# Kernel tuning notes

Measured on AMD Instinct MI355X. Metric: run time of the kernel, lower is better.

The kernel has to match this reference:

```python
import jax, jax.numpy as jnp
import numpy as np

B, C, HID, H, W_ = 16, 2048, 256, 32, 32

def setup_inputs() -> dict:
    key = jax.random.key(0)
    k1, k2, k3 = jax.random.split(key, 3)
    return {
        "query_features": jax.random.normal(k1, (B, C, H, W_), dtype=jnp.float32),
        "prompt_features": jax.random.normal(k2, (B, C, H, W_), dtype=jnp.float32),
        "W": jax.random.normal(k3, (HID, C), dtype=jnp.float32) * 0.02,
        "b": jnp.zeros((HID,), dtype=jnp.float32),
    }

def reference(query_features, prompt_features, W, b):
    Bq, Cc, Hh, Ww = query_features.shape
    HW = Hh * Ww
    # 1x1 conv == channel matmul
    Q = jnp.einsum('oc,bchw->bohw', W, query_features) + b[None, :, None, None]
    K = jnp.einsum('oc,bchw->bohw', W, prompt_features) + b[None, :, None, None]
    Qf = Q.reshape(Bq, -1, HW)          # (b, hid, HW1)
    Kf = K.reshape(Bq, -1, HW)          # (b, hid, HW2)
    Vf = prompt_features.reshape(Bq, Cc, HW)  # (b, C, HW2)
    scores = jnp.einsum('bcq,bck->bqk', Qf, Kf)   # (b, HW1, HW2)
    A = jax.nn.softmax(scores, axis=-1)
    aligned = jnp.einsum('bqk,bck->bcq', A, Vf).reshape(Bq, Cc, Hh, Ww)
    # fusion_policy == 'cat'
    return jnp.concatenate([query_features, aligned], axis=1)
```

## Files before the change

kernel.cpp:

```cpp
#include <hip/hip_runtime.h>

#define NB   16
#define NC   2048
#define NHID 256
#define NHW  1024
#define ROWH 36

using half4_t  = __attribute__((ext_vector_type(4))) _Float16;
using half8_t  = __attribute__((ext_vector_type(8))) _Float16;
using float4_t = __attribute__((ext_vector_type(4))) float;

__global__ __launch_bounds__(256) void copy_kernel(const uint4* __restrict__ qf,
                                                   uint4* __restrict__ out) {
    int idx = blockIdx.x * 256 + threadIdx.x;
    int b = idx >> 19;
    int r = idx & 0x7FFFF;
    out[((size_t)b << 20) + r] = qf[idx];
}

__device__ __forceinline__ void stage_f32(const float* __restrict__ src, size_t stride,
                                          int k0, _Float16* __restrict__ dst, int t) {
    #pragma unroll
    for (int i = 0; i < 4; ++i) {
        int flat = i * 256 + t;
        int row = flat >> 3;
        int ch  = flat & 7;
        float4 v = *(const float4*)(src + (size_t)row * stride + k0 + ch * 4);
        half4_t h;
        h[0] = (_Float16)v.x; h[1] = (_Float16)v.y;
        h[2] = (_Float16)v.z; h[3] = (_Float16)v.w;
        *(half4_t*)(dst + row * ROWH + ch * 4) = h;
    }
}

__device__ __forceinline__ void stage_f16(const _Float16* __restrict__ src, size_t stride,
                                          int k0, _Float16* __restrict__ dst, int t) {
    #pragma unroll
    for (int i = 0; i < 2; ++i) {
        int flat = i * 256 + t;
        int row = flat >> 2;
        int ch  = flat & 3;
        const _Float16* p = src + (size_t)row * stride + k0 + ch * 8;
        half4_t h0 = *(const half4_t*)p;
        half4_t h1 = *(const half4_t*)(p + 4);
        *(half4_t*)(dst + row * ROWH + ch * 8)     = h0;
        *(half4_t*)(dst + row * ROWH + ch * 8 + 4) = h1;
    }
}

__device__ __forceinline__ void stage_f32_T(const float* __restrict__ src, size_t stride,
                                            int k0, _Float16* __restrict__ dst, int t) {
    const int j = t & 31;
    const int g = t >> 5;
    float4 xr[4];
    #pragma unroll
    for (int r = 0; r < 4; ++r)
        xr[r] = *(const float4*)(src + (size_t)(k0 + g * 4 + r) * stride + j * 4);
    #pragma unroll
    for (int e = 0; e < 4; ++e) {
        half4_t h;
        h[0] = (_Float16)((&xr[0].x)[e]);
        h[1] = (_Float16)((&xr[1].x)[e]);
        h[2] = (_Float16)((&xr[2].x)[e]);
        h[3] = (_Float16)((&xr[3].x)[e]);
        *(half4_t*)(dst + (j * 4 + e) * ROWH + g * 4) = h;
    }
}

__device__ __forceinline__ void mfma_step(const _Float16* __restrict__ As,
                                          const _Float16* __restrict__ Bs,
                                          int wr, int wc, int quad, int l15,
                                          float4_t acc[4][4]) {
    half8_t af[4], bf[4];
    #pragma unroll
    for (int i = 0; i < 4; ++i) {
        const _Float16* pa = As + (wr + i * 16 + l15) * ROWH + quad * 8;
        half4_t a0 = *(const half4_t*)pa;
        half4_t a1 = *(const half4_t*)(pa + 4);
        const _Float16* pb = Bs + (wc + i * 16 + l15) * ROWH + quad * 8;
        half4_t b0 = *(const half4_t*)pb;
        half4_t b1 = *(const half4_t*)(pb + 4);
        #pragma unroll
        for (int e = 0; e < 4; ++e) {
            af[i][e] = a0[e]; af[i][4 + e] = a1[e];
            bf[i][e] = b0[e]; bf[i][4 + e] = b1[e];
        }
    }
    #pragma unroll
    for (int i = 0; i < 4; ++i)
        #pragma unroll
        for (int j = 0; j < 4; ++j)
            acc[i][j] = __builtin_amdgcn_mfma_f32_16x16x32_f16(af[i], bf[j], acc[i][j], 0, 0, 0);
}

#define ACC_INIT(acc) \
    _Pragma("unroll") for (int i_ = 0; i_ < 4; ++i_) \
    _Pragma("unroll") for (int j_ = 0; j_ < 4; ++j_) \
    _Pragma("unroll") for (int r_ = 0; r_ < 4; ++r_) acc[i_][j_][r_] = 0.f;

__global__ __launch_bounds__(256) void proj16_kernel(
    const float* __restrict__ qf, const float* __restrict__ pf,
    const float* __restrict__ Wm, const float* __restrict__ bias,
    _Float16* __restrict__ Q16, _Float16* __restrict__ K16)
{
    __shared__ _Float16 As[128 * ROWH];
    __shared__ _Float16 Bs[128 * ROWH];
    const int z = blockIdx.z;
    const int which = z >> 4;
    const int b = z & 15;
    const float* X = (which ? pf : qf) + (size_t)b * NC * NHW;
    _Float16* O = (which ? K16 : Q16) + (size_t)b * NHW * NHID;
    const int m0 = blockIdx.y * 128;
    const int n0 = blockIdx.x * 128;
    const int t = threadIdx.x;
    const int w = t >> 6, l = t & 63, quad = l >> 4, l15 = l & 15;
    const int wr = (w >> 1) * 64, wc = (w & 1) * 64;

    float4_t acc[4][4];
    ACC_INIT(acc)

    for (int k0 = 0; k0 < NC; k0 += 32) {
        stage_f32_T(X + m0, NHW, k0, As, t);
        stage_f32(Wm + (size_t)n0 * NC, NC, k0, Bs, t);
        __syncthreads();
        mfma_step(As, Bs, wr, wc, quad, l15, acc);
        __syncthreads();
    }
    float bv[4];
    #pragma unroll
    for (int j = 0; j < 4; ++j) bv[j] = bias[n0 + wc + j * 16 + l15];
    #pragma unroll
    for (int i = 0; i < 4; ++i)
        #pragma unroll
        for (int j = 0; j < 4; ++j)
            #pragma unroll
            for (int r = 0; r < 4; ++r) {
                int hw  = m0 + wr + i * 16 + quad * 4 + r;
                int hid = n0 + wc + j * 16 + l15;
                O[(size_t)hw * NHID + hid] = (_Float16)(acc[i][j][r] + bv[j]);
            }
}

__global__ __launch_bounds__(256) void scores16_kernel(
    const _Float16* __restrict__ Q16, const _Float16* __restrict__ K16,
    float* __restrict__ S)
{
    __shared__ _Float16 As[128 * ROWH];
    __shared__ _Float16 Bs[128 * ROWH];
    const int b = blockIdx.z;
    const _Float16* Qb = Q16 + (size_t)b * NHW * NHID;
    const _Float16* Kb = K16 + (size_t)b * NHW * NHID;
    float* Sb = S + (size_t)b * NHW * NHW;
    const int m0 = blockIdx.y * 128;
    const int n0 = blockIdx.x * 128;
    const int t = threadIdx.x;
    const int w = t >> 6, l = t & 63, quad = l >> 4, l15 = l & 15;
    const int wr = (w >> 1) * 64, wc = (w & 1) * 64;

    float4_t acc[4][4];
    ACC_INIT(acc)

    for (int k0 = 0; k0 < NHID; k0 += 32) {
        stage_f16(Qb + (size_t)m0 * NHID, NHID, k0, As, t);
        stage_f16(Kb + (size_t)n0 * NHID, NHID, k0, Bs, t);
        __syncthreads();
        mfma_step(As, Bs, wr, wc, quad, l15, acc);
        __syncthreads();
    }
    #pragma unroll
    for (int i = 0; i < 4; ++i)
        #pragma unroll
        for (int j = 0; j < 4; ++j)
            #pragma unroll
            for (int r = 0; r < 4; ++r) {
                int q1 = m0 + wr + i * 16 + quad * 4 + r;
                int q2 = n0 + wc + j * 16 + l15;
                Sb[(size_t)q1 * NHW + q2] = acc[i][j][r];
            }
}

__global__ __launch_bounds__(256) void softmax_kernel(float* __restrict__ S) {
    const int t = threadIdx.x;
    const int wave = t >> 6;
    const int lane = t & 63;
    float* row = S + ((size_t)blockIdx.x * 4 + wave) * NHW;

    float4 v[4];
    float mx = -1e30f;
    #pragma unroll
    for (int j = 0; j < 4; ++j) {
        v[j] = *(const float4*)(row + (lane << 2) + (j << 8));
        mx = fmaxf(mx, fmaxf(fmaxf(v[j].x, v[j].y), fmaxf(v[j].z, v[j].w)));
    }
    #pragma unroll
    for (int off = 32; off >= 1; off >>= 1)
        mx = fmaxf(mx, __shfl_xor(mx, off, 64));

    float s = 0.f;
    #pragma unroll
    for (int j = 0; j < 4; ++j) {
        v[j].x = __expf(v[j].x - mx); v[j].y = __expf(v[j].y - mx);
        v[j].z = __expf(v[j].z - mx); v[j].w = __expf(v[j].w - mx);
        s += v[j].x + v[j].y + v[j].z + v[j].w;
    }
    #pragma unroll
    for (int off = 32; off >= 1; off >>= 1)
        s += __shfl_xor(s, off, 64);

    const float inv = 1.0f / s;
    #pragma unroll
    for (int j = 0; j < 4; ++j) {
        v[j].x *= inv; v[j].y *= inv; v[j].z *= inv; v[j].w *= inv;
        *(float4*)(row + (lane << 2) + (j << 8)) = v[j];
    }
}

__global__ __launch_bounds__(256) void av16_kernel(
    const float* __restrict__ pf, const float* __restrict__ S,
    float* __restrict__ out)
{
    __shared__ _Float16 As[128 * ROWH];
    __shared__ _Float16 Bs[128 * ROWH];
    const int b = blockIdx.z;
    const float* Vb = pf + (size_t)b * NC * NHW;
    const float* Ab = S + (size_t)b * NHW * NHW;
    float* Ob = out + (size_t)b * (2 * NC) * NHW + (size_t)NC * NHW;
    const int m0 = blockIdx.y * 128;
    const int n0 = blockIdx.x * 128;
    const int t = threadIdx.x;
    const int w = t >> 6, l = t & 63, quad = l >> 4, l15 = l & 15;
    const int wr = (w >> 1) * 64, wc = (w & 1) * 64;

    float4_t acc[4][4];
    ACC_INIT(acc)

    for (int k0 = 0; k0 < NHW; k0 += 32) {
        stage_f32(Vb + (size_t)m0 * NHW, NHW, k0, As, t);
        stage_f32(Ab + (size_t)n0 * NHW, NHW, k0, Bs, t);
        __syncthreads();
        mfma_step(As, Bs, wr, wc, quad, l15, acc);
        __syncthreads();
    }
    #pragma unroll
    for (int i = 0; i < 4; ++i)
        #pragma unroll
        for (int j = 0; j < 4; ++j)
            #pragma unroll
            for (int r = 0; r < 4; ++r) {
                int c = m0 + wr + i * 16 + quad * 4 + r;
                int q = n0 + wc + j * 16 + l15;
                Ob[(size_t)c * NHW + q] = acc[i][j][r];
            }
}

extern "C" void kernel_launch(void* const* d_in, const int* in_sizes, int n_in,
                              void* d_out, int out_size, void* d_ws, size_t ws_size,
                              hipStream_t stream) {
    const float* qf   = (const float*)d_in[0];
    const float* pf   = (const float*)d_in[1];
    const float* Wm   = (const float*)d_in[2];
    const float* bias = (const float*)d_in[3];
    float* out = (float*)d_out;

    copy_kernel<<<32768, 256, 0, stream>>>((const uint4*)qf, (uint4*)out);

    const size_t q16elems = (size_t)NB * NHW * NHID;
    _Float16* Q16 = (_Float16*)d_ws;
    _Float16* K16 = Q16 + q16elems;
    float* S = (float*)((char*)d_ws + 2 * q16elems * sizeof(_Float16));

    proj16_kernel<<<dim3(2, 8, 32), 256, 0, stream>>>(qf, pf, Wm, bias, Q16, K16);
    scores16_kernel<<<dim3(8, 8, 16), 256, 0, stream>>>(Q16, K16, S);
    softmax_kernel<<<NB * 256, 256, 0, stream>>>(S);
    av16_kernel<<<dim3(8, 16, 16), 256, 0, stream>>>(pf, S, out);
}
```

Measured before the change: 707.8 us.

## Pre-convert inputs to fp16, use async LDS loads with swizzle, fp16 softmax output

Adds a prep kernel that converts query and prompt features to fp16. It writes them transposed (hw-major) into workspace and into the output buffer as scratch, and also stores V in fp16, so the GEMMs no longer convert fp32 on the fly. The weight matrix is pre-converted to fp16. All GEMMs now share one routine that uses global_load_lds async copies into an XOR-swizzled LDS tile with K-step 64. Softmax writes fp16 probabilities in place, the AV GEMM reads those fp16 probabilities and fp16 V, and the copy of the query features into the output runs last to overwrite the scratch. This trades extra conversion passes and output-buffer aliasing for halved GEMM operand bandwidth and cheaper staging.

```diff
diff --git a/kernel.cpp b/kernel.cpp
--- a/kernel.cpp
+++ b/kernel.cpp
@@ -4,11 +4,237 @@
 #define NC   2048
 #define NHID 256
 #define NHW  1024
-#define ROWH 36
 
 using half4_t  = __attribute__((ext_vector_type(4))) _Float16;
 using half8_t  = __attribute__((ext_vector_type(8))) _Float16;
 using float4_t = __attribute__((ext_vector_type(4))) float;
+
+#define OUT_BATCH_BYTES ((size_t)(4096u * 1024u) * 4u)
+
+__device__ __forceinline__ void async_load16(const void* g, void* l) {
+    __builtin_amdgcn_global_load_lds((__attribute__((address_space(1))) void*)g,
+                                     (__attribute__((address_space(3))) void*)l, 16, 0, 0);
+}
+
+__device__ __forceinline__ void stage_async(const _Float16* __restrict__ src, size_t stride_h,
+                                            _Float16* __restrict__ lds, int t) {
+    #pragma unroll
+    for (int i = 0; i < 4; ++i) {
+        const int o   = i * 4096 + t * 16;
+        const int row = o >> 7;
+        const int s   = ((o >> 4) & 7) ^ (row & 7);
+        const _Float16* g = src + (size_t)row * stride_h + s * 8;
+        async_load16(g, (char*)lds + o);
+    }
+}
+
+__device__ __forceinline__ half8_t frag_read(const _Float16* __restrict__ lds, int row, int kk, int quad) {
+    const int s = (kk * 4 + quad) ^ (row & 7);
+    return *(const half8_t*)((const char*)lds + row * 128 + s * 16);
+}
+
+#define ACC_INIT(acc) \
+    _Pragma("unroll") for (int i_ = 0; i_ < 4; ++i_) \
+    _Pragma("unroll") for (int j_ = 0; j_ < 4; ++j_) \
+    _Pragma("unroll") for (int r_ = 0; r_ < 4; ++r_) acc[i_][j_][r_] = 0.f;
+
+__device__ __forceinline__ void gemm_f16(const _Float16* __restrict__ A, size_t lda,
+                                         const _Float16* __restrict__ B, size_t ldb,
+                                         int K, _Float16* __restrict__ As, _Float16* __restrict__ Bs,
+                                         float4_t acc[4][4]) {
+    const int t = threadIdx.x;
+    const int l = t & 63, quad = l >> 4, l15 = l & 15;
+    const int w = t >> 6;
+    const int wr = (w >> 1) * 64, wc = (w & 1) * 64;
+    for (int k0 = 0; k0 < K; k0 += 64) {
+        stage_async(A + k0, lda, As, t);
+        stage_async(B + k0, ldb, Bs, t);
+        __syncthreads();
+        #pragma unroll
+        for (int kk = 0; kk < 2; ++kk) {
+            half8_t af[4], bf[4];
+            #pragma unroll
+            for (int i = 0; i < 4; ++i) af[i] = frag_read(As, wr + i * 16 + l15, kk, quad);
+            #pragma unroll
+            for (int j = 0; j < 4; ++j) bf[j] = frag_read(Bs, wc + j * 16 + l15, kk, quad);
+            #pragma unroll
+            for (int i = 0; i < 4; ++i)
+                #pragma unroll
+                for (int j = 0; j < 4; ++j)
+                    acc[i][j] = __builtin_amdgcn_mfma_f32_16x16x32_f16(af[i], bf[j], acc[i][j], 0, 0, 0);
+        }
+        __syncthreads();
+    }
+}
+
+__global__ __launch_bounds__(256) void prep_kernel(
+    const float* __restrict__ qf, const float* __restrict__ pf,
+    _Float16* __restrict__ qT, float* __restrict__ out) {
+    __shared__ _Float16 tile[64][72];
+    const int z = blockIdx.z, which = z >> 4, b = z & 15;
+    const int c0 = blockIdx.y * 64, h0 = blockIdx.x * 64;
+    const float* X = (which ? pf : qf) + (size_t)b * NC * NHW;
+    _Float16* T = which ? (_Float16*)((char*)out + (size_t)b * OUT_BATCH_BYTES + (4u << 20))
+                        : (qT + (size_t)b * NHW * NC);
+    const int t = threadIdx.x;
+    const int row = t >> 2, seg = t & 3;
+    const float* src = X + (size_t)(c0 + row) * NHW + h0 + seg * 16;
+    float4 v[4];
+    #pragma unroll
+    for (int i = 0; i < 4; ++i) v[i] = *(const float4*)(src + i * 4);
+    half8_t h[2];
+    #pragma unroll
+    for (int i = 0; i < 2; ++i) {
+        #pragma unroll
+        for (int e = 0; e < 4; ++e) {
+            h[i][e]     = (_Float16)((&v[2 * i].x)[e]);
+            h[i][4 + e] = (_Float16)((&v[2 * i + 1].x)[e]);
+        }
+        *(half8_t*)&tile[row][seg * 16 + i * 8] = h[i];
+    }
+    if (which) {
+        _Float16* vd = (_Float16*)((char*)out + (size_t)b * OUT_BATCH_BYTES)
+                       + (size_t)(c0 + row) * NHW + h0 + seg * 16;
+        *(half8_t*)vd = h[0];
+        *(half8_t*)(vd + 8) = h[1];
+    }
+    __syncthreads();
+    const int hr = t >> 2;
+    half8_t o[2];
+    #pragma unroll
+    for (int i = 0; i < 2; ++i)
+        #pragma unroll
+        for (int e = 0; e < 8; ++e) o[i][e] = tile[seg * 16 + i * 8 + e][hr];
+    _Float16* od = T + (size_t)(h0 + hr) * NC + c0 + seg * 16;
+    *(half8_t*)od = o[0];
+    *(half8_t*)(od + 8) = o[1];
+}
+
+__global__ __launch_bounds__(256) void wcvt_kernel(const float* __restrict__ W, _Float16* __restrict__ W16) {
+    const int idx = (blockIdx.x * 256 + threadIdx.x) * 8;
+    float4 a = *(const float4*)(W + idx);
+    float4 c = *(const float4*)(W + idx + 4);
+    half8_t h;
+    h[0] = (_Float16)a.x; h[1] = (_Float16)a.y; h[2] = (_Float16)a.z; h[3] = (_Float16)a.w;
+    h[4] = (_Float16)c.x; h[5] = (_Float16)c.y; h[6] = (_Float16)c.z; h[7] = (_Float16)c.w;
+    *(half8_t*)(W16 + idx) = h;
+}
+
+__global__ __launch_bounds__(256) void proj16_kernel(
+    const _Float16* __restrict__ qT, const float* __restrict__ out_scratch,
+    const _Float16* __restrict__ W16, const float* __restrict__ bias,
+    _Float16* __restrict__ Q16, _Float16* __restrict__ K16) {
+    __shared__ __attribute__((aligned(16))) _Float16 As[8192];
+    __shared__ __attribute__((aligned(16))) _Float16 Bs[8192];
+    const int z = blockIdx.z, which = z >> 4, b = z & 15;
+    const _Float16* X = which
+        ? (const _Float16*)((const char*)out_scratch + (size_t)b * OUT_BATCH_BYTES + (4u << 20))
+        : (qT + (size_t)b * NHW * NC);
+    _Float16* O = (which ? K16 : Q16) + (size_t)b * NHW * NHID;
+    const int m0 = blockIdx.y * 128, n0 = blockIdx.x * 128;
+    float4_t acc[4][4];
+    ACC_INIT(acc)
+    gemm_f16(X + (size_t)m0 * NC, NC, W16 + (size_t)n0 * NC, NC, NC, As, Bs, acc);
+    const int t = threadIdx.x, l = t & 63, quad = l >> 4, l15 = l & 15, w = t >> 6;
+    const int wr = (w >> 1) * 64, wc = (w & 1) * 64;
+    #pragma unroll
+    for (int j = 0; j < 4; ++j) {
+        const float bv = bias[n0 + wc + j * 16 + l15];
+        #pragma unroll
+        for (int i = 0; i < 4; ++i)
+            #pragma unroll
+            for (int r = 0; r < 4; ++r) {
+                int hw  = m0 + wr + i * 16 + quad * 4 + r;
+                int hid = n0 + wc + j * 16 + l15;
+                O[(size_t)hw * NHID + hid] = (_Float16)(acc[i][j][r] + bv);
+            }
+    }
+}
+
+__global__ __launch_bounds__(256) void scores16_kernel(
+    const _Float16* __restrict__ Q16, const _Float16* __restrict__ K16, float* __restrict__ S) {
+    __shared__ __attribute__((aligned(16))) _Float16 As[8192];
+    __shared__ __attribute__((aligned(16))) _Float16 Bs[8192];
+    const int b = blockIdx.z;
+    const int m0 = blockIdx.y * 128, n0 = blockIdx.x * 128;
+    float* Sb = S + (size_t)b * NHW * NHW;
+    float4_t acc[4][4];
+    ACC_INIT(acc)
+    gemm_f16(Q16 + (size_t)b * NHW * NHID + (size_t)m0 * NHID, NHID,
+             K16 + (size_t)b * NHW * NHID + (size_t)n0 * NHID, NHID, NHID, As, Bs, acc);
+    const int t = threadIdx.x, l = t & 63, quad = l >> 4, l15 = l & 15, w = t >> 6;
+    const int wr = (w >> 1) * 64, wc = (w & 1) * 64;
+    #pragma unroll
+    for (int i = 0; i < 4; ++i)
+        #pragma unroll
+        for (int j = 0; j < 4; ++j)
+            #pragma unroll
+            for (int r = 0; r < 4; ++r) {
+                int q1 = m0 + wr + i * 16 + quad * 4 + r;
+                int q2 = n0 + wc + j * 16 + l15;
+                Sb[(size_t)q1 * NHW + q2] = acc[i][j][r];
+            }
+}
+
+__global__ __launch_bounds__(256) void softmax_kernel(float* __restrict__ S) {
+    const int t = threadIdx.x, wave = t >> 6, lane = t & 63;
+    float* row = S + ((size_t)blockIdx.x * 4 + wave) * NHW;
+    float4 v[4];
+    float mx = -1e30f;
+    #pragma unroll
+    for (int j = 0; j < 4; ++j) {
+        v[j] = *(const float4*)(row + (lane << 2) + (j << 8));
+        mx = fmaxf(mx, fmaxf(fmaxf(v[j].x, v[j].y), fmaxf(v[j].z, v[j].w)));
+    }
+    #pragma unroll
+    for (int off = 32; off >= 1; off >>= 1) mx = fmaxf(mx, __shfl_xor(mx, off, 64));
+    float s = 0.f;
+    #pragma unroll
+    for (int j = 0; j < 4; ++j) {
+        v[j].x = __expf(v[j].x - mx); v[j].y = __expf(v[j].y - mx);
+        v[j].z = __expf(v[j].z - mx); v[j].w = __expf(v[j].w - mx);
+        s += v[j].x + v[j].y + v[j].z + v[j].w;
+    }
+    #pragma unroll
+    for (int off = 32; off >= 1; off >>= 1) s += __shfl_xor(s, off, 64);
+    const float inv = 1.0f / s;
+    __syncthreads();
+    _Float16* o = (_Float16*)row;
+    #pragma unroll
+    for (int j = 0; j < 4; ++j) {
+        half4_t h;
+        h[0] = (_Float16)(v[j].x * inv); h[1] = (_Float16)(v[j].y * inv);
+        h[2] = (_Float16)(v[j].z * inv); h[3] = (_Float16)(v[j].w * inv);
+        *(half4_t*)(o + (lane << 2) + (j << 8)) = h;
+    }
+}
+
+__global__ __launch_bounds__(256) void av16_kernel(
+    const float* __restrict__ S, float* __restrict__ out) {
+    __shared__ __attribute__((aligned(16))) _Float16 As[8192];
+    __shared__ __attribute__((aligned(16))) _Float16 Bs[8192];
+    const int b = blockIdx.z;
+    const _Float16* Vb  = (const _Float16*)((const char*)out + (size_t)b * OUT_BATCH_BYTES);
+    const _Float16* A16 = (const _Float16*)(S + (size_t)b * NHW * NHW);
+    float* Ob = out + (size_t)b * (2 * NC) * NHW + (size_t)NC * NHW;
+    const int m0 = blockIdx.y * 128;
+    const int n0 = blockIdx.x * 128;
+    float4_t acc[4][4];
+    ACC_INIT(acc)
+    gemm_f16(Vb + (size_t)m0 * NHW, NHW, A16 + (size_t)n0 * 2048, 2048, NHW, As, Bs, acc);
+    const int t = threadIdx.x, l = t & 63, quad = l >> 4, l15 = l & 15, w = t >> 6;
+    const int wr = (w >> 1) * 64, wc = (w & 1) * 64;
+    #pragma unroll
+    for (int i = 0; i < 4; ++i)
+        #pragma unroll
+        for (int j = 0; j < 4; ++j)
+            #pragma unroll
+            for (int r = 0; r < 4; ++r) {
+                int c = m0 + wr + i * 16 + quad * 4 + r;
+                int q = n0 + wc + j * 16 + l15;
+                Ob[(size_t)c * NHW + q] = acc[i][j][r];
+            }
+}
 
 __global__ __launch_bounds__(256) void copy_kernel(const uint4* __restrict__ qf,
                                                    uint4* __restrict__ out) {
@@ -16,241 +242,6 @@
     int b = idx >> 19;
     int r = idx & 0x7FFFF;
     out[((size_t)b << 20) + r] = qf[idx];
-}
-
-__device__ __forceinline__ void stage_f32(const float* __restrict__ src, size_t stride,
-                                          int k0, _Float16* __restrict__ dst, int t) {
-    #pragma unroll
-    for (int i = 0; i < 4; ++i) {
-        int flat = i * 256 + t;
-        int row = flat >> 3;
-        int ch  = flat & 7;
-        float4 v = *(const float4*)(src + (size_t)row * stride + k0 + ch * 4);
-        half4_t h;
-        h[0] = (_Float16)v.x; h[1] = (_Float16)v.y;
-        h[2] = (_Float16)v.z; h[3] = (_Float16)v.w;
-        *(half4_t*)(dst + row * ROWH + ch * 4) = h;
-    }
-}
-
-__device__ __forceinline__ void stage_f16(const _Float16* __restrict__ src, size_t stride,
-                                          int k0, _Float16* __restrict__ dst, int t) {
-    #pragma unroll
-    for (int i = 0; i < 2; ++i) {
-        int flat = i * 256 + t;
-        int row = flat >> 2;
-        int ch  = flat & 3;
-        const _Float16* p = src + (size_t)row * stride + k0 + ch * 8;
-        half4_t h0 = *(const half4_t*)p;
-        half4_t h1 = *(const half4_t*)(p + 4);
-        *(half4_t*)(dst + row * ROWH + ch * 8)     = h0;
-        *(half4_t*)(dst + row * ROWH + ch * 8 + 4) = h1;
-    }
-}
-
-__device__ __forceinline__ void stage_f32_T(const float* __restrict__ src, size_t stride,
-                                            int k0, _Float16* __restrict__ dst, int t) {
-    const int j = t & 31;
-    const int g = t >> 5;
-    float4 xr[4];
-    #pragma unroll
-    for (int r = 0; r < 4; ++r)
-        xr[r] = *(const float4*)(src + (size_t)(k0 + g * 4 + r) * stride + j * 4);
-    #pragma unroll
-    for (int e = 0; e < 4; ++e) {
-        half4_t h;
-        h[0] = (_Float16)((&xr[0].x)[e]);
-        h[1] = (_Float16)((&xr[1].x)[e]);
-        h[2] = (_Float16)((&xr[2].x)[e]);
-        h[3] = (_Float16)((&xr[3].x)[e]);
-        *(half4_t*)(dst + (j * 4 + e) * ROWH + g * 4) = h;
-    }
-}
-
-__device__ __forceinline__ void mfma_step(const _Float16* __restrict__ As,
-                                          const _Float16* __restrict__ Bs,
-                                          int wr, int wc, int quad, int l15,
-                                          float4_t acc[4][4]) {
-    half8_t af[4], bf[4];
-    #pragma unroll
-    for (int i = 0; i < 4; ++i) {
-        const _Float16* pa = As + (wr + i * 16 + l15) * ROWH + quad * 8;
-        half4_t a0 = *(const half4_t*)pa;
-        half4_t a1 = *(const half4_t*)(pa + 4);
-        const _Float16* pb = Bs + (wc + i * 16 + l15) * ROWH + quad * 8;
-        half4_t b0 = *(const half4_t*)pb;
-        half4_t b1 = *(const half4_t*)(pb + 4);
-        #pragma unroll
-        for (int e = 0; e < 4; ++e) {
-            af[i][e] = a0[e]; af[i][4 + e] = a1[e];
-            bf[i][e] = b0[e]; bf[i][4 + e] = b1[e];
-        }
-    }
-    #pragma unroll
-    for (int i = 0; i < 4; ++i)
-        #pragma unroll
-        for (int j = 0; j < 4; ++j)
-            acc[i][j] = __builtin_amdgcn_mfma_f32_16x16x32_f16(af[i], bf[j], acc[i][j], 0, 0, 0);
-}
-
-#define ACC_INIT(acc) \
-    _Pragma("unroll") for (int i_ = 0; i_ < 4; ++i_) \
-    _Pragma("unroll") for (int j_ = 0; j_ < 4; ++j_) \
-    _Pragma("unroll") for (int r_ = 0; r_ < 4; ++r_) acc[i_][j_][r_] = 0.f;
-
-__global__ __launch_bounds__(256) void proj16_kernel(
-    const float* __restrict__ qf, const float* __restrict__ pf,
-    const float* __restrict__ Wm, const float* __restrict__ bias,
-    _Float16* __restrict__ Q16, _Float16* __restrict__ K16)
-{
-    __shared__ _Float16 As[128 * ROWH];
-    __shared__ _Float16 Bs[128 * ROWH];
-    const int z = blockIdx.z;
-    const int which = z >> 4;
-    const int b = z & 15;
-    const float* X = (which ? pf : qf) + (size_t)b * NC * NHW;
-    _Float16* O = (which ? K16 : Q16) + (size_t)b * NHW * NHID;
-    const int m0 = blockIdx.y * 128;
-    const int n0 = blockIdx.x * 128;
-    const int t = threadIdx.x;
-    const int w = t >> 6, l = t & 63, quad = l >> 4, l15 = l & 15;
-    const int wr = (w >> 1) * 64, wc = (w & 1) * 64;
-
-    float4_t acc[4][4];
-    ACC_INIT(acc)
-
-    for (int k0 = 0; k0 < NC; k0 += 32) {
-        stage_f32_T(X + m0, NHW, k0, As, t);
-        stage_f32(Wm + (size_t)n0 * NC, NC, k0, Bs, t);
-        __syncthreads();
-        mfma_step(As, Bs, wr, wc, quad, l15, acc);
-        __syncthreads();
-    }
-    float bv[4];
-    #pragma unroll
-    for (int j = 0; j < 4; ++j) bv[j] = bias[n0 + wc + j * 16 + l15];
-    #pragma unroll
-    for (int i = 0; i < 4; ++i)
-        #pragma unroll
-        for (int j = 0; j < 4; ++j)
-            #pragma unroll
-            for (int r = 0; r < 4; ++r) {
-                int hw  = m0 + wr + i * 16 + quad * 4 + r;
-                int hid = n0 + wc + j * 16 + l15;
-                O[(size_t)hw * NHID + hid] = (_Float16)(acc[i][j][r] + bv[j]);
-            }
-}
-
-__global__ __launch_bounds__(256) void scores16_kernel(
-    const _Float16* __restrict__ Q16, const _Float16* __restrict__ K16,
-    float* __restrict__ S)
-{
-    __shared__ _Float16 As[128 * ROWH];
-    __shared__ _Float16 Bs[128 * ROWH];
-    const int b = blockIdx.z;
-    const _Float16* Qb = Q16 + (size_t)b * NHW * NHID;
-    const _Float16* Kb = K16 + (size_t)b * NHW * NHID;
-    float* Sb = S + (size_t)b * NHW * NHW;
-    const int m0 = blockIdx.y * 128;
-    const int n0 = blockIdx.x * 128;
-    const int t = threadIdx.x;
-    const int w = t >> 6, l = t & 63, quad = l >> 4, l15 = l & 15;
-    const int wr = (w >> 1) * 64, wc = (w & 1) * 64;
-
-    float4_t acc[4][4];
-    ACC_INIT(acc)
-
-    for (int k0 = 0; k0 < NHID; k0 += 32) {
-        stage_f16(Qb + (size_t)m0 * NHID, NHID, k0, As, t);
-        stage_f16(Kb + (size_t)n0 * NHID, NHID, k0, Bs, t);
-        __syncthreads();
-        mfma_step(As, Bs, wr, wc, quad, l15, acc);
-        __syncthreads();
-    }
-    #pragma unroll
-    for (int i = 0; i < 4; ++i)
-        #pragma unroll
-        for (int j = 0; j < 4; ++j)
-            #pragma unroll
-            for (int r = 0; r < 4; ++r) {
-                int q1 = m0 + wr + i * 16 + quad * 4 + r;
-                int q2 = n0 + wc + j * 16 + l15;
-                Sb[(size_t)q1 * NHW + q2] = acc[i][j][r];
-            }
-}
-
-__global__ __launch_bounds__(256) void softmax_kernel(float* __restrict__ S) {
-    const int t = threadIdx.x;
-    const int wave = t >> 6;
-    const int lane = t & 63;
-    float* row = S + ((size_t)blockIdx.x * 4 + wave) * NHW;
-
-    float4 v[4];
-    float mx = -1e30f;
-    #pragma unroll
-    for (int j = 0; j < 4; ++j) {
-        v[j] = *(const float4*)(row + (lane << 2) + (j << 8));
-        mx = fmaxf(mx, fmaxf(fmaxf(v[j].x, v[j].y), fmaxf(v[j].z, v[j].w)));
-    }
-    #pragma unroll
-    for (int off = 32; off >= 1; off >>= 1)
-        mx = fmaxf(mx, __shfl_xor(mx, off, 64));
-
-    float s = 0.f;
-    #pragma unroll
-    for (int j = 0; j < 4; ++j) {
-        v[j].x = __expf(v[j].x - mx); v[j].y = __expf(v[j].y - mx);
-        v[j].z = __expf(v[j].z - mx); v[j].w = __expf(v[j].w - mx);
-        s += v[j].x + v[j].y + v[j].z + v[j].w;
-    }
-    #pragma unroll
-    for (int off = 32; off >= 1; off >>= 1)
-        s += __shfl_xor(s, off, 64);
-
-    const float inv = 1.0f / s;
-    #pragma unroll
-    for (int j = 0; j < 4; ++j) {
-        v[j].x *= inv; v[j].y *= inv; v[j].z *= inv; v[j].w *= inv;
-        *(float4*)(row + (lane << 2) + (j << 8)) = v[j];
-    }
-}
-
-__global__ __launch_bounds__(256) void av16_kernel(
-    const float* __restrict__ pf, const float* __restrict__ S,
-    float* __restrict__ out)
-{
-    __shared__ _Float16 As[128 * ROWH];
-    __shared__ _Float16 Bs[128 * ROWH];
-    const int b = blockIdx.z;
-    const float* Vb = pf + (size_t)b * NC * NHW;
-    const float* Ab = S + (size_t)b * NHW * NHW;
-    float* Ob = out + (size_t)b * (2 * NC) * NHW + (size_t)NC * NHW;
-    const int m0 = blockIdx.y * 128;
-    const int n0 = blockIdx.x * 128;
-    const int t = threadIdx.x;
-    const int w = t >> 6, l = t & 63, quad = l >> 4, l15 = l & 15;
-    const int wr = (w >> 1) * 64, wc = (w & 1) * 64;
-
-    float4_t acc[4][4];
-    ACC_INIT(acc)
-
-    for (int k0 = 0; k0 < NHW; k0 += 32) {
-        stage_f32(Vb + (size_t)m0 * NHW, NHW, k0, As, t);
-        stage_f32(Ab + (size_t)n0 * NHW, NHW, k0, Bs, t);
-        __syncthreads();
-        mfma_step(As, Bs, wr, wc, quad, l15, acc);
-        __syncthreads();
-    }
-    #pragma unroll
-    for (int i = 0; i < 4; ++i)
-        #pragma unroll
-        for (int j = 0; j < 4; ++j)
-            #pragma unroll
-            for (int r = 0; r < 4; ++r) {
-                int c = m0 + wr + i * 16 + quad * 4 + r;
-                int q = n0 + wc + j * 16 + l15;
-                Ob[(size_t)c * NHW + q] = acc[i][j][r];
-            }
 }
 
 extern "C" void kernel_launch(void* const* d_in, const int* in_sizes, int n_in,
@@ -262,15 +253,17 @@
     const float* bias = (const float*)d_in[3];
     float* out = (float*)d_out;
 
-    copy_kernel<<<32768, 256, 0, stream>>>((const uint4*)qf, (uint4*)out);
-
-    const size_t q16elems = (size_t)NB * NHW * NHID;
-    _Float16* Q16 = (_Float16*)d_ws;
-    _Float16* K16 = Q16 + q16elems;
-    float* S = (float*)((char*)d_ws + 2 * q16elems * sizeof(_Float16));
-
-    proj16_kernel<<<dim3(2, 8, 32), 256, 0, stream>>>(qf, pf, Wm, bias, Q16, K16);
+    _Float16* qT  = (_Float16*)d_ws;
+    float*    S   = (float*)d_ws;
+    _Float16* Q16 = (_Float16*)((char*)d_ws + ((size_t)64 << 20));
+    _Float16* K16 = (_Float16*)((char*)d_ws + ((size_t)72 << 20));
+    _Float16* W16 = (_Float16*)((char*)out + ((size_t)8 << 20));
+
+    prep_kernel<<<dim3(16, 32, 32), 256, 0, stream>>>(qf, pf, qT, out);
+    wcvt_kernel<<<256, 256, 0, stream>>>(Wm, W16);
+    proj16_kernel<<<dim3(2, 8, 32), 256, 0, stream>>>(qT, out, W16, bias, Q16, K16);
     scores16_kernel<<<dim3(8, 8, 16), 256, 0, stream>>>(Q16, K16, S);
     softmax_kernel<<<NB * 256, 256, 0, stream>>>(S);
-    av16_kernel<<<dim3(8, 16, 16), 256, 0, stream>>>(pf, S, out);
-}
+    av16_kernel<<<dim3(8, 16, 16), 256, 0, stream>>>(S, out);
+    copy_kernel<<<32768, 256, 0, stream>>>((const uint4*)qf, (uint4*)out);
+}
```

After: 692.6 us. 1.02x faster.
